# Kernel tuning notes

Measured on AMD Instinct MI355X. Metric: run time of the kernel, lower is better.

The kernel has to match this reference:

```python
import jax, jax.numpy as jnp
import numpy as np

N = 50000
E = 800000
F_IN = 500
H = 5          # heads
C = 32         # per-head channels
HID = H * C    # 160
NC = 20        # num_classes
G = 8          # number of graphs in batch
SLOPE_ATT = 0.2   # GATConv attention leaky slope (PyG default)
SLOPE_ACT = 0.01  # F.leaky_relu default


def _layernorm(x, scale, bias, eps=1e-5):
    mu = jnp.mean(x, axis=-1, keepdims=True)
    var = jnp.var(x, axis=-1, keepdims=True)
    return (x - mu) * jax.lax.rsqrt(var + eps) * scale + bias


def _edge_softmax(logits, dst, num_nodes):
    # segment softmax over incoming edges of each destination node
    m = jax.ops.segment_max(logits, dst, num_segments=num_nodes)
    ex = jnp.exp(logits - m[dst])
    s = jax.ops.segment_sum(ex, dst, num_segments=num_nodes)
    return ex / (s[dst] + 1e-16)


def _gat_layer(x, src, dst, W, a_src, a_dst, b):
    n = x.shape[0]
    h = (x @ W).reshape(n, H, C)                       # [N,H,C]
    al_s = jnp.einsum('nhc,hc->nh', h, a_src)          # [N,H]
    al_d = jnp.einsum('nhc,hc->nh', h, a_dst)
    logits = jax.nn.leaky_relu(al_s[src] + al_d[dst], SLOPE_ATT)  # [Et,H]
    alpha = _edge_softmax(logits, dst, n)              # [Et,H]
    msg = h[src] * alpha[..., None]                    # [Et,H,C]
    out = jax.ops.segment_sum(msg, dst, num_segments=n).reshape(n, HID) + b
    return out, alpha


def setup_inputs():
    key = jax.random.key(0)
    ks = jax.random.split(key, 24)
    p = lambda k, shp: jax.random.normal(k, shp, jnp.float32) * 0.05
    x = jax.random.normal(ks[0], (N, F_IN), jnp.float32)
    edge_index = jax.random.randint(ks[1], (2, E), 0, N, jnp.int64)
    batch = jnp.sort(jax.random.randint(ks[2], (N,), 0, G, jnp.int64))
    return {
        'x': x, 'edge_index': edge_index, 'batch': batch,
        'W1': p(ks[3], (F_IN, HID)), 'a_src1': p(ks[4], (H, C)), 'a_dst1': p(ks[5], (H, C)), 'b1': jnp.zeros((HID,), jnp.float32),
        'ln1_s': jnp.ones((HID,), jnp.float32), 'ln1_b': jnp.zeros((HID,), jnp.float32),
        'W2': p(ks[6], (HID, HID)), 'a_src2': p(ks[7], (H, C)), 'a_dst2': p(ks[8], (H, C)), 'b2': jnp.zeros((HID,), jnp.float32),
        'ln2_s': jnp.ones((HID,), jnp.float32), 'ln2_b': jnp.zeros((HID,), jnp.float32),
        'Wm': p(ks[9], (HID, HID)), 'bm': jnp.zeros((HID,), jnp.float32),
        'Wmlp1': p(ks[10], (HID, HID)), 'bmlp1': jnp.zeros((HID,), jnp.float32),
        'ln3_s': jnp.ones((HID,), jnp.float32), 'ln3_b': jnp.zeros((HID,), jnp.float32),
        'Wmlp2': p(ks[11], (HID, NC)), 'bmlp2': jnp.zeros((NC,), jnp.float32),
    }


def reference(x, edge_index, batch, W1, a_src1, a_dst1, b1, ln1_s, ln1_b,
              W2, a_src2, a_dst2, b2, ln2_s, ln2_b, Wm, bm,
              Wmlp1, bmlp1, ln3_s, ln3_b, Wmlp2, bmlp2):
    n = x.shape[0]
    # PyG GATConv adds self-loops by default
    loops = jnp.arange(n, dtype=edge_index.dtype)
    src = jnp.concatenate([edge_index[0], loops])
    dst = jnp.concatenate([edge_index[1], loops])

    h1, alpha1 = _gat_layer(x, src, dst, W1, a_src1, a_dst1, b1)
    h1 = jax.nn.leaky_relu(h1, SLOPE_ACT)
    h1 = _layernorm(h1, ln1_s, ln1_b)      # dropout = identity at eval

    h2, alpha2 = _gat_layer(h1, src, dst, W2, a_src2, a_dst2, b2)
    h2 = jax.nn.leaky_relu(h2, SLOPE_ACT)
    h2 = _layernorm(h2, ln2_s, ln2_b)

    xo = jax.nn.leaky_relu(h2 @ Wm + bm, SLOPE_ACT)   # [N,HID]

    # global_mean_pool over batch assignment
    sums = jax.ops.segment_sum(xo, batch, num_segments=G)
    cnts = jax.ops.segment_sum(jnp.ones((n, 1), xo.dtype), batch, num_segments=G)
    pooled = sums / jnp.maximum(cnts, 1.0)            # [G,HID]

    z = pooled @ Wmlp1 + bmlp1
    z = jax.nn.relu(_layernorm(z, ln3_s, ln3_b))
    rec = z @ Wmlp2 + bmlp2                           # [G,NC]
    return xo, rec, alpha1, alpha2
```

## Files before the change

kernel.cpp:

```cpp
#include <hip/hip_runtime.h>
#include <hip/hip_bf16.h>
#include <cstdint>
#include <cstddef>

#define NN   50000
#define EE   800000
#define ET_  (EE + NN)
#define FIN  500
#define HID_ 160
#define NC_  20
#define GG   8

typedef __attribute__((ext_vector_type(8))) short ab8;
typedef __attribute__((ext_vector_type(4))) float f4;

static __device__ __forceinline__ unsigned short f2bf(float v) {
    union { float f; uint32_t u; } c; c.f = v;
    uint32_t r = c.u + 0x7FFFu + ((c.u >> 16) & 1u);
    return (unsigned short)(r >> 16);
}

static __device__ __forceinline__ float2 bf2f2(uint32_t u) {
    union { uint32_t u; float f; } a, b;
    a.u = u << 16;
    b.u = u & 0xffff0000u;
    return make_float2(a.f, b.f);
}

static __device__ __forceinline__ int lbound_i(const int* arr, int n, int val) {
    int lo = 0, hi = n;
    while (lo < hi) { int mid = (lo + hi) >> 1; if (arr[mid] < val) lo = mid + 1; else hi = mid; }
    return lo;
}

__global__ __launch_bounds__(256) void k_hist(const int* __restrict__ ei, int* __restrict__ deg) {
    int e = blockIdx.x * 256 + threadIdx.x;
    if (e >= ET_) return;
    int d = (e < EE) ? ei[EE + e] : (e - EE);
    atomicAdd(&deg[d], 1);
}

__global__ __launch_bounds__(256) void k_scan1(const int* __restrict__ deg, int* __restrict__ rowptr,
                                               int* __restrict__ bsum) {
    __shared__ int s[256];
    int t = threadIdx.x;
    int base = blockIdx.x * 1024 + t * 4;
    int v0 = (base + 0 < NN) ? deg[base + 0] : 0;
    int v1 = (base + 1 < NN) ? deg[base + 1] : 0;
    int v2 = (base + 2 < NN) ? deg[base + 2] : 0;
    int v3 = (base + 3 < NN) ? deg[base + 3] : 0;
    int tot = v0 + v1 + v2 + v3;
    s[t] = tot;
    __syncthreads();
    for (int off = 1; off < 256; off <<= 1) {
        int y = (t >= off) ? s[t - off] : 0;
        __syncthreads();
        s[t] += y;
        __syncthreads();
    }
    int excl = s[t] - tot;
    if (t == 255) bsum[blockIdx.x] = s[255];
    if (base + 0 < NN) rowptr[base + 0] = excl;  excl += v0;
    if (base + 1 < NN) rowptr[base + 1] = excl;  excl += v1;
    if (base + 2 < NN) rowptr[base + 2] = excl;  excl += v2;
    if (base + 3 < NN) rowptr[base + 3] = excl;
}

__global__ void k_scan2(int* __restrict__ bsum, int nb) {
    int t = threadIdx.x;
    int v = (t < nb) ? bsum[t] : 0;
    int orig = v;
    for (int off = 1; off < 64; off <<= 1) {
        int y = __shfl_up(v, off);
        if (t >= off) v += y;
    }
    if (t < nb) bsum[t] = v - orig;
}

__global__ __launch_bounds__(256) void k_scan3(int* __restrict__ rowptr, const int* __restrict__ bsum,
                                               int* __restrict__ cursor) {
    int i = blockIdx.x * 256 + threadIdx.x;
    if (i < NN) {
        int r = rowptr[i] + bsum[i >> 10];
        rowptr[i] = r;
        cursor[i] = r;
    }
    if (i == NN) rowptr[NN] = ET_;
}

__global__ __launch_bounds__(256) void k_scatter(const int* __restrict__ ei, int* __restrict__ cursor,
                                                 int2* __restrict__ epair) {
    int e = blockIdx.x * 256 + threadIdx.x;
    if (e >= ET_) return;
    int s, d;
    if (e < EE) { s = ei[e]; d = ei[EE + e]; } else { s = e - EE; d = e - EE; }
    int slot = atomicAdd(&cursor[d], 1);
    epair[slot] = make_int2(e, s);
}

__global__ __launch_bounds__(256) void k_prep_all(const float* __restrict__ W1, unsigned short* __restrict__ Wt1,
                                                  const float* __restrict__ W2, unsigned short* __restrict__ Wt2,
                                                  const float* __restrict__ Wm, unsigned short* __restrict__ Wmt,
                                                  float* __restrict__ pooled) {
    int idx = blockIdx.x * 256 + threadIdx.x;
    const int S1 = HID_ * 512, S2 = HID_ * HID_;
    if (idx < GG * HID_) pooled[idx] = 0.f;
    if (idx < S1) {
        int n = idx / 512, k = idx - n * 512;
        Wt1[idx] = (k < FIN) ? f2bf(W1[(size_t)k * HID_ + n]) : (unsigned short)0;
    } else if (idx < S1 + S2) {
        int j = idx - S1;
        int n = j / HID_, k = j - n * HID_;
        Wt2[j] = f2bf(W2[(size_t)k * HID_ + n]);
    } else if (idx < S1 + 2 * S2) {
        int j = idx - S1 - S2;
        int n = j / HID_, k = j - n * HID_;
        Wmt[j] = f2bf(Wm[(size_t)k * HID_ + n]);
    }
}

template<int ABF>
static __device__ __forceinline__ void gemm_body(const void* __restrict__ Av,
                                                 const unsigned short* __restrict__ Bt,
                                                 float* __restrict__ C, __hip_bfloat16* __restrict__ Cb,
                                                 int M, int K, int Kp,
                                                 const float* __restrict__ bias, int act,
                                                 const float* __restrict__ asrc, const float* __restrict__ adst,
                                                 float* __restrict__ als_o, float* __restrict__ ald_o,
                                                 const int* __restrict__ batch_p, float* __restrict__ pooled) {
    int tid  = threadIdx.x;
    int lane = tid & 63;
    int w    = tid >> 6;
    int fr   = lane & 15;
    int q    = lane >> 4;
    int row0 = blockIdx.x * 64;
    int arow = row0 + w * 16 + fr;
    bool rv  = arow < M;

    f4 acc[10];
#pragma unroll
    for (int t = 0; t < 10; t++) acc[t] = (f4)0.f;

    const int nk = Kp >> 5;
    const unsigned short* bbase = Bt + (size_t)fr * Kp + q * 8;

    auto loadA = [&](int s) -> ab8 {
        ab8 a = (ab8)0;
        int k0 = s * 32 + q * 8;
        if (ABF) {
            const unsigned short* Ab = (const unsigned short*)Av;
            if (rv) a = *reinterpret_cast<const ab8*>(&Ab[(size_t)arow * K + k0]);
        } else {
            const float* A = (const float*)Av;
            if (rv && k0 + 8 <= K) {
                const float4* s4 = reinterpret_cast<const float4*>(&A[(size_t)arow * K + k0]);
                float4 u = s4[0], v = s4[1];
                unsigned short pk[8] = {f2bf(u.x), f2bf(u.y), f2bf(u.z), f2bf(u.w),
                                        f2bf(v.x), f2bf(v.y), f2bf(v.z), f2bf(v.w)};
                a = *reinterpret_cast<ab8*>(pk);
            } else if (rv && k0 < K) {
                unsigned short pk[8];
#pragma unroll
                for (int c = 0; c < 8; c++)
                    pk[c] = (k0 + c < K) ? f2bf(A[(size_t)arow * K + k0 + c]) : (unsigned short)0;
                a = *reinterpret_cast<ab8*>(pk);
            }
        }
        return a;
    };

    ab8 acur = loadA(0);
    for (int s = 0; s < nk; s++) {
        ab8 anx = (ab8)0;
        if (s + 1 < nk) anx = loadA(s + 1);
        const unsigned short* bp = bbase + (size_t)s * 32;
#pragma unroll
        for (int t = 0; t < 10; t++) {
            ab8 b = *reinterpret_cast<const ab8*>(&bp[(size_t)t * 16 * Kp]);
            acc[t] = __builtin_amdgcn_mfma_f32_16x16x32_bf16(acur, b, acc[t], 0, 0, 0);
        }
        acur = anx;
    }

    if (als_o) {
        float av_s[10], av_d[10];
#pragma unroll
        for (int t = 0; t < 10; t++) { av_s[t] = asrc[t * 16 + fr]; av_d[t] = adst[t * 16 + fr]; }
#pragma unroll
        for (int i = 0; i < 4; i++) {
            int r = row0 + w * 16 + q * 4 + i;
            float ps[5], pd[5];
#pragma unroll
            for (int h = 0; h < 5; h++) {
                ps[h] = acc[2 * h][i] * av_s[2 * h] + acc[2 * h + 1][i] * av_s[2 * h + 1];
                pd[h] = acc[2 * h][i] * av_d[2 * h] + acc[2 * h + 1][i] * av_d[2 * h + 1];
            }
#pragma unroll
            for (int off = 8; off >= 1; off >>= 1)
#pragma unroll
                for (int h = 0; h < 5; h++) {
                    ps[h] += __shfl_xor(ps[h], off);
                    pd[h] += __shfl_xor(pd[h], off);
                }
            if (fr == 0 && r < M) {
#pragma unroll
                for (int h = 0; h < 5; h++) {
                    als_o[(size_t)r * 5 + h] = ps[h];
                    ald_o[(size_t)r * 5 + h] = pd[h];
                }
            }
        }
    }

    int gu = -2;
    if (pooled) {
        int rhi = row0 + 63; if (rhi >= M) rhi = M - 1;
        int gl = batch_p[row0], gh = batch_p[rhi];
        gu = (gl == gh) ? gl : -1;
    }
    float psum[10];
#pragma unroll
    for (int t = 0; t < 10; t++) psum[t] = 0.f;

    int rbase = row0 + w * 16 + q * 4;
#pragma unroll
    for (int t = 0; t < 10; t++) {
        int col = t * 16 + fr;
        float bv = bias ? bias[col] : 0.f;
#pragma unroll
        for (int i = 0; i < 4; i++) {
            int r = rbase + i;
            float v = acc[t][i] + bv;
            if (act) v = v > 0.f ? v : 0.01f * v;
            if (r < M) {
                if (C)  C[(size_t)r * HID_ + col] = v;
                if (Cb) *reinterpret_cast<unsigned short*>(&Cb[(size_t)r * HID_ + col]) = f2bf(v);
                if (gu >= 0) psum[t] += v;
                else if (gu == -1) atomicAdd(&pooled[batch_p[r] * HID_ + col], v);
            }
        }
    }
    if (gu >= 0) {
#pragma unroll
        for (int t = 0; t < 10; t++) {
            psum[t] += __shfl_xor(psum[t], 16);
            psum[t] += __shfl_xor(psum[t], 32);
        }
        if (q == 0) {
#pragma unroll
            for (int t = 0; t < 10; t++)
                atomicAdd(&pooled[gu * HID_ + t * 16 + fr], psum[t]);
        }
    }
}

__global__ __launch_bounds__(256) void k_gemm_f32(const void* __restrict__ Av,
                                                  const unsigned short* __restrict__ Bt,
                                                  float* __restrict__ C, __hip_bfloat16* __restrict__ Cb,
                                                  int M, int K, int Kp,
                                                  const float* __restrict__ bias, int act,
                                                  const float* __restrict__ asrc, const float* __restrict__ adst,
                                                  float* __restrict__ als_o, float* __restrict__ ald_o,
                                                  const int* __restrict__ batch_p, float* __restrict__ pooled) {
    gemm_body<0>(Av, Bt, C, Cb, M, K, Kp, bias, act, asrc, adst, als_o, ald_o, batch_p, pooled);
}

__global__ __launch_bounds__(256) void k_gemm_bf16(const void* __restrict__ Av,
                                                   const unsigned short* __restrict__ Bt,
                                                   float* __restrict__ C, __hip_bfloat16* __restrict__ Cb,
                                                   int M, int K, int Kp,
                                                   const float* __restrict__ bias, int act,
                                                   const float* __restrict__ asrc, const float* __restrict__ adst,
                                                   float* __restrict__ als_o, float* __restrict__ ald_o,
                                                   const int* __restrict__ batch_p, float* __restrict__ pooled) {
    gemm_body<1>(Av, Bt, C, Cb, M, K, Kp, bias, act, asrc, adst, als_o, ald_o, batch_p, pooled);
}

__global__ __launch_bounds__(256) void k_att_agg(const int* __restrict__ rowptr,
                                                 const int2* __restrict__ epair,
                                                 const float* __restrict__ als, const float* __restrict__ ald,
                                                 const __hip_bfloat16* __restrict__ hmat,
                                                 float* __restrict__ alphap,
                                                 float* __restrict__ alpha_out,
                                                 const float* __restrict__ bias,
                                                 const float* __restrict__ lns, const float* __restrict__ lnb,
                                                 __hip_bfloat16* __restrict__ outb) {
    __shared__ float sExp[4][64 * 5];
    __shared__ int2  sPair[4][64];
    int wv   = threadIdx.x >> 6;
    int lane = threadIdx.x & 63;
    int node = blockIdx.x * 4 + wv;
    if (node >= NN) return;
    int start = rowptr[node], end = rowptr[node + 1];
    int deg = end - start;
    bool fits = (deg <= 64);
    float ad[5];
#pragma unroll
    for (int h = 0; h < 5; h++) ad[h] = ald[node * 5 + h];

    float sm[5] = {0.f, 0.f, 0.f, 0.f, 0.f};
    for (int j = start + lane; j < end; j += 64) {
        int2 p = epair[j];
        const float* as = &als[(size_t)p.y * 5];
        int idx = j - start;
        if (fits) sPair[wv][idx] = p;
#pragma unroll
        for (int h = 0; h < 5; h++) {
            float l = as[h] + ad[h];
            l = l > 0.f ? l : 0.2f * l;
            float ex = __expf(fminf(l, 60.f));
            sm[h] += ex;
            if (fits) sExp[wv][idx * 5 + h] = ex;
            else      alphap[(size_t)j * 5 + h] = ex;
        }
    }
#pragma unroll
    for (int off = 32; off >= 1; off >>= 1)
#pragma unroll
        for (int h = 0; h < 5; h++) sm[h] += __shfl_xor(sm[h], off);
    float inv[5];
#pragma unroll
    for (int h = 0; h < 5; h++) inv[h] = 1.f / (sm[h] + 1e-16f);

    int h0 = lane >> 4;
    bool lo16 = lane < 16;
    int c01 = 2 * lane;
    int c2  = 128 + 2 * lane;
    float2 A  = make_float2(0.f, 0.f), B2 = make_float2(0.f, 0.f);
    float2 A2 = make_float2(0.f, 0.f), B22 = make_float2(0.f, 0.f);

    if (fits) {
        if (lane < deg) {
            int2 p = sPair[wv][lane];
            float* ao = &alpha_out[(size_t)p.x * 5];
#pragma unroll
            for (int h = 0; h < 5; h++) ao[h] = sExp[wv][lane * 5 + h] * inv[h];
        }
        int idx = 0;
        for (; idx + 1 < deg; idx += 2) {
            int sA = sPair[wv][idx].y, sB = sPair[wv][idx + 1].y;
            float wA = sExp[wv][idx * 5 + h0] * inv[h0];
            float wB = sExp[wv][(idx + 1) * 5 + h0] * inv[h0];
            const unsigned short* rA = (const unsigned short*)&hmat[(size_t)sA * HID_];
            const unsigned short* rB = (const unsigned short*)&hmat[(size_t)sB * HID_];
            float2 fA = bf2f2(*reinterpret_cast<const uint32_t*>(&rA[c01]));
            float2 fB = bf2f2(*reinterpret_cast<const uint32_t*>(&rB[c01]));
            A.x += wA * fA.x; A.y += wA * fA.y;
            B2.x += wB * fB.x; B2.y += wB * fB.y;
            if (lo16) {
                float wA4 = sExp[wv][idx * 5 + 4] * inv[4];
                float wB4 = sExp[wv][(idx + 1) * 5 + 4] * inv[4];
                float2 gA = bf2f2(*reinterpret_cast<const uint32_t*>(&rA[c2]));
                float2 gB = bf2f2(*reinterpret_cast<const uint32_t*>(&rB[c2]));
                A2.x += wA4 * gA.x; A2.y += wA4 * gA.y;
                B22.x += wB4 * gB.x; B22.y += wB4 * gB.y;
            }
        }
        if (idx < deg) {
            int sA = sPair[wv][idx].y;
            float wA = sExp[wv][idx * 5 + h0] * inv[h0];
            const unsigned short* rA = (const unsigned short*)&hmat[(size_t)sA * HID_];
            float2 fA = bf2f2(*reinterpret_cast<const uint32_t*>(&rA[c01]));
            A.x += wA * fA.x; A.y += wA * fA.y;
            if (lo16) {
                float wA4 = sExp[wv][idx * 5 + 4] * inv[4];
                float2 gA = bf2f2(*reinterpret_cast<const uint32_t*>(&rA[c2]));
                A2.x += wA4 * gA.x; A2.y += wA4 * gA.y;
            }
        }
    } else {
        for (int j = start + lane; j < end; j += 64) {
            int2 p = epair[j];
            float* ao = &alpha_out[(size_t)p.x * 5];
#pragma unroll
            for (int h = 0; h < 5; h++) ao[h] = alphap[(size_t)j * 5 + h] * inv[h];
        }
        for (int j = start; j < end; j++) {
            int2 p = epair[j];
            const float* ap = &alphap[(size_t)j * 5];
            float wA = ap[h0] * inv[h0];
            const unsigned short* rA = (const unsigned short*)&hmat[(size_t)p.y * HID_];
            float2 fA = bf2f2(*reinterpret_cast<const uint32_t*>(&rA[c01]));
            A.x += wA * fA.x; A.y += wA * fA.y;
            if (lo16) {
                float wA4 = ap[4] * inv[4];
                float2 gA = bf2f2(*reinterpret_cast<const uint32_t*>(&rA[c2]));
                A2.x += wA4 * gA.x; A2.y += wA4 * gA.y;
            }
        }
    }
    A.x += B2.x; A.y += B2.y; A2.x += B22.x; A2.y += B22.y;

    float2 bb = *reinterpret_cast<const float2*>(&bias[c01]);
    float v0 = A.x + bb.x;  v0 = v0 > 0.f ? v0 : 0.01f * v0;
    float v1 = A.y + bb.y;  v1 = v1 > 0.f ? v1 : 0.01f * v1;
    float v2 = 0.f, v3 = 0.f;
    if (lo16) {
        float2 b2 = *reinterpret_cast<const float2*>(&bias[c2]);
        v2 = A2.x + b2.x; v2 = v2 > 0.f ? v2 : 0.01f * v2;
        v3 = A2.y + b2.y; v3 = v3 > 0.f ? v3 : 0.01f * v3;
    }
    float s  = v0 + v1 + v2 + v3;
    float sq = v0 * v0 + v1 * v1 + v2 * v2 + v3 * v3;
#pragma unroll
    for (int off = 32; off >= 1; off >>= 1) {
        s  += __shfl_xor(s, off);
        sq += __shfl_xor(sq, off);
    }
    float m = s * (1.f / 160.f);
    float r = rsqrtf(sq * (1.f / 160.f) - m * m + 1e-5f);
    size_t ob = (size_t)node * HID_;
    {
        float2 sc = *reinterpret_cast<const float2*>(&lns[c01]);
        float2 bi = *reinterpret_cast<const float2*>(&lnb[c01]);
        uint32_t pk = (uint32_t)f2bf((v0 - m) * r * sc.x + bi.x)
                    | ((uint32_t)f2bf((v1 - m) * r * sc.y + bi.y) << 16);
        *reinterpret_cast<uint32_t*>(&outb[ob + c01]) = pk;
    }
    if (lo16) {
        float2 sc = *reinterpret_cast<const float2*>(&lns[c2]);
        float2 bi = *reinterpret_cast<const float2*>(&lnb[c2]);
        uint32_t pk = (uint32_t)f2bf((v2 - m) * r * sc.x + bi.x)
                    | ((uint32_t)f2bf((v3 - m) * r * sc.y + bi.y) << 16);
        *reinterpret_cast<uint32_t*>(&outb[ob + c2]) = pk;
    }
}

__global__ __launch_bounds__(256) void k_mlp(const float* __restrict__ pooled, const int* __restrict__ batch,
                                             const float* __restrict__ W1, const float* __restrict__ b1,
                                             const float* __restrict__ lns, const float* __restrict__ lnb,
                                             const float* __restrict__ W2, const float* __restrict__ b2,
                                             float* __restrict__ rec) {
    __shared__ float P[GG][HID_];
    __shared__ float Z[GG][HID_];
    __shared__ float mu[GG], rr[GG], ic[GG];
    int t = threadIdx.x;
    if (t < GG) {
        int lo = lbound_i(batch, NN, t), hi = lbound_i(batch, NN, t + 1);
        ic[t] = 1.f / fmaxf((float)(hi - lo), 1.f);
    }
    __syncthreads();
    for (int i = t; i < GG * HID_; i += 256) P[i / HID_][i % HID_] = pooled[i] * ic[i / HID_];
    __syncthreads();
    for (int i = t; i < GG * HID_; i += 256) {
        int g = i / HID_, j = i % HID_;
        float acc = b1[j];
        for (int k = 0; k < HID_; k++) acc += P[g][k] * W1[k * HID_ + j];
        Z[g][j] = acc;
    }
    __syncthreads();
    if (t < GG) {
        float s = 0.f, sq = 0.f;
        for (int k = 0; k < HID_; k++) { float z = Z[t][k]; s += z; sq += z * z; }
        float m = s / (float)HID_;
        mu[t] = m;
        rr[t] = rsqrtf(sq / (float)HID_ - m * m + 1e-5f);
    }
    __syncthreads();
    for (int i = t; i < GG * HID_; i += 256) {
        int g = i / HID_, j = i % HID_;
        float z = (Z[g][j] - mu[g]) * rr[g] * lns[j] + lnb[j];
        Z[g][j] = fmaxf(z, 0.f);
    }
    __syncthreads();
    for (int i = t; i < GG * NC_; i += 256) {
        int g = i / NC_, j = i % NC_;
        float acc = b2[j];
        for (int k = 0; k < HID_; k++) acc += Z[g][k] * W2[k * NC_ + j];
        rec[g * NC_ + j] = acc;
    }
}

extern "C" void kernel_launch(void* const* d_in, const int* in_sizes, int n_in,
                              void* d_out, int out_size, void* d_ws, size_t ws_size,
                              hipStream_t stream) {
    const float* x    = (const float*)d_in[0];
    const int*   ei   = (const int*)d_in[1];
    const int*   batch= (const int*)d_in[2];
    const float* W1   = (const float*)d_in[3];
    const float* as1  = (const float*)d_in[4];
    const float* ad1  = (const float*)d_in[5];
    const float* b1   = (const float*)d_in[6];
    const float* ln1s = (const float*)d_in[7];
    const float* ln1b = (const float*)d_in[8];
    const float* W2   = (const float*)d_in[9];
    const float* as2  = (const float*)d_in[10];
    const float* ad2  = (const float*)d_in[11];
    const float* b2   = (const float*)d_in[12];
    const float* ln2s = (const float*)d_in[13];
    const float* ln2b = (const float*)d_in[14];
    const float* Wm   = (const float*)d_in[15];
    const float* bm   = (const float*)d_in[16];
    const float* Wm1  = (const float*)d_in[17];
    const float* bm1  = (const float*)d_in[18];
    const float* ln3s = (const float*)d_in[19];
    const float* ln3b = (const float*)d_in[20];
    const float* Wm2  = (const float*)d_in[21];
    const float* bm2  = (const float*)d_in[22];

    float* out    = (float*)d_out;
    float* xo     = out;
    float* rec    = out + (size_t)NN * HID_;
    float* alpha1 = rec + GG * NC_;
    float* alpha2 = alpha1 + (size_t)ET_ * 5;

    char* w = (char*)d_ws;
    auto carve = [&](size_t bytes) { char* p = w; w += (bytes + 255) & ~(size_t)255; return p; };
    int*   deg    = (int*)carve((size_t)NN * 4);
    int*   rowptr = (int*)carve((size_t)(NN + 1) * 4);
    int*   cursor = (int*)carve((size_t)NN * 4);
    int2*  epair  = (int2*)carve((size_t)ET_ * 8);
    int*   bsum   = (int*)carve(64 * 4);
    __hip_bfloat16* hbuf  = (__hip_bfloat16*)carve((size_t)NN * HID_ * 2);
    __hip_bfloat16* xbufb = (__hip_bfloat16*)carve((size_t)NN * HID_ * 2);
    float* alphap = (float*)carve((size_t)ET_ * 5 * 4);
    float* als    = (float*)carve((size_t)NN * 5 * 4);
    float* ald    = (float*)carve((size_t)NN * 5 * 4);
    float* pooled = (float*)carve((size_t)GG * HID_ * 4);
    unsigned short* Wt1 = (unsigned short*)carve((size_t)HID_ * 512 * 2);
    unsigned short* Wt2 = (unsigned short*)carve((size_t)HID_ * HID_ * 2);
    unsigned short* Wmt = (unsigned short*)carve((size_t)HID_ * HID_ * 2);

    hipMemsetAsync(deg, 0, (size_t)NN * 4, stream);
    k_hist<<<(ET_ + 255) / 256, 256, 0, stream>>>(ei, deg);
    int nb = (NN + 1023) / 1024;
    k_scan1<<<nb, 256, 0, stream>>>(deg, rowptr, bsum);
    k_scan2<<<1, 64, 0, stream>>>(bsum, nb);
    k_scan3<<<(NN + 1 + 255) / 256, 256, 0, stream>>>(rowptr, bsum, cursor);
    k_scatter<<<(ET_ + 255) / 256, 256, 0, stream>>>(ei, cursor, epair);

    const int PREP = HID_ * 512 + 2 * HID_ * HID_;
    k_prep_all<<<(PREP + 255) / 256, 256, 0, stream>>>(W1, Wt1, W2, Wt2, Wm, Wmt, pooled);

    const int NWB = (NN + 3) / 4;
    const int GB  = (NN + 63) / 64;

    k_gemm_f32<<<GB, 256, 0, stream>>>(x, Wt1, nullptr, hbuf, NN, FIN, 512, nullptr, 0,
                                       as1, ad1, als, ald, nullptr, nullptr);
    k_att_agg<<<NWB, 256, 0, stream>>>(rowptr, epair, als, ald, hbuf, alphap, alpha1,
                                       b1, ln1s, ln1b, xbufb);

    k_gemm_bf16<<<GB, 256, 0, stream>>>(xbufb, Wt2, nullptr, hbuf, NN, HID_, HID_, nullptr, 0,
                                        as2, ad2, als, ald, nullptr, nullptr);
    k_att_agg<<<NWB, 256, 0, stream>>>(rowptr, epair, als, ald, hbuf, alphap, alpha2,
                                       b2, ln2s, ln2b, xbufb);

    k_gemm_bf16<<<GB, 256, 0, stream>>>(xbufb, Wmt, xo, nullptr, NN, HID_, HID_, bm, 1,
                                        nullptr, nullptr, nullptr, nullptr, batch, pooled);
    k_mlp<<<1, 256, 0, stream>>>(pooled, batch, Wm1, bm1, ln3s, ln3b, Wm2, bm2, rec);
}
```

Baseline: 717.0 us.

## Pre-pack weights and input into MFMA fragment order with deeper prefetch

Weights are repacked into MFMA fragment order so each lane does one coalesced 16-byte load per tile. The fp32 input x is converted to bf16 in a separate kernel, also in fragment order, staged in the output buffer. The GEMM main loop now double-buffers B fragments in registers and prefetches A two steps ahead. This removes strided B loads and in-loop fp32 conversion, but adds an extra pass over x, register pressure and a scratch dependency on d_out before xo is written.

```diff
diff --git a/kernel.cpp b/kernel.cpp
--- a/kernel.cpp
+++ b/kernel.cpp
@@ -10,6 +10,9 @@
 #define HID_ 160
 #define NC_  20
 #define GG   8
+#define GB1  ((NN + 63) / 64)
+#define NK1  16
+#define NK2  5
 
 typedef __attribute__((ext_vector_type(8))) short ab8;
 typedef __attribute__((ext_vector_type(4))) float f4;
@@ -98,32 +101,64 @@
     epair[slot] = make_int2(e, s);
 }
 
-__global__ __launch_bounds__(256) void k_prep_all(const float* __restrict__ W1, unsigned short* __restrict__ Wt1,
-                                                  const float* __restrict__ W2, unsigned short* __restrict__ Wt2,
-                                                  const float* __restrict__ Wm, unsigned short* __restrict__ Wmt,
+__global__ __launch_bounds__(256) void k_prep_all(const float* __restrict__ W1, ab8* __restrict__ B1,
+                                                  const float* __restrict__ W2, ab8* __restrict__ B2,
+                                                  const float* __restrict__ Wm, ab8* __restrict__ Bm,
                                                   float* __restrict__ pooled) {
     int idx = blockIdx.x * 256 + threadIdx.x;
-    const int S1 = HID_ * 512, S2 = HID_ * HID_;
     if (idx < GG * HID_) pooled[idx] = 0.f;
-    if (idx < S1) {
-        int n = idx / 512, k = idx - n * 512;
-        Wt1[idx] = (k < FIN) ? f2bf(W1[(size_t)k * HID_ + n]) : (unsigned short)0;
-    } else if (idx < S1 + S2) {
-        int j = idx - S1;
-        int n = j / HID_, k = j - n * HID_;
-        Wt2[j] = f2bf(W2[(size_t)k * HID_ + n]);
-    } else if (idx < S1 + 2 * S2) {
-        int j = idx - S1 - S2;
-        int n = j / HID_, k = j - n * HID_;
-        Wmt[j] = f2bf(Wm[(size_t)k * HID_ + n]);
-    }
-}
-
-template<int ABF>
+    const int C1 = NK1 * 10 * 64;
+    const int C2 = NK2 * 10 * 64;
+    const float* W; ab8* Bo; int K, cidx;
+    if (idx < C1)                { W = W1; Bo = B1; K = FIN;  cidx = idx; }
+    else if (idx < C1 + C2)      { W = W2; Bo = B2; K = HID_; cidx = idx - C1; }
+    else if (idx < C1 + 2 * C2)  { W = Wm; Bo = Bm; K = HID_; cidx = idx - C1 - C2; }
+    else return;
+    int s = cidx / 640, r = cidx % 640;
+    int t = r >> 6, l = r & 63;
+    int fr = l & 15, q = l >> 4;
+    int n  = t * 16 + fr;
+    int k0 = s * 32 + q * 8;
+    unsigned short pk[8];
+#pragma unroll
+    for (int j = 0; j < 8; j++) {
+        int k = k0 + j;
+        pk[j] = (k < K) ? f2bf(W[(size_t)k * HID_ + n]) : (unsigned short)0;
+    }
+    Bo[cidx] = *reinterpret_cast<ab8*>(pk);
+}
+
+__global__ __launch_bounds__(256) void k_conv_x(const float* __restrict__ x, ab8* __restrict__ Apk) {
+    int idx = blockIdx.x * 256 + threadIdx.x;
+    int tid = idx & 255;
+    int s   = (idx >> 8) & (NK1 - 1);
+    int blk = idx >> 12;
+    int l = tid & 63, w = tid >> 6;
+    int fr = l & 15, q = l >> 4;
+    int row = blk * 64 + w * 16 + fr;
+    int k0 = s * 32 + q * 8;
+    unsigned short pk[8] = {0, 0, 0, 0, 0, 0, 0, 0};
+    if (row < NN) {
+        const float* xr = &x[(size_t)row * FIN];
+        if (k0 + 8 <= FIN) {
+            const float4* s4 = reinterpret_cast<const float4*>(&xr[k0]);
+            float4 u = s4[0], v = s4[1];
+            pk[0] = f2bf(u.x); pk[1] = f2bf(u.y); pk[2] = f2bf(u.z); pk[3] = f2bf(u.w);
+            pk[4] = f2bf(v.x); pk[5] = f2bf(v.y); pk[6] = f2bf(v.z); pk[7] = f2bf(v.w);
+        } else {
+#pragma unroll
+            for (int j = 0; j < 8; j++)
+                if (k0 + j < FIN) pk[j] = f2bf(xr[k0 + j]);
+        }
+    }
+    Apk[idx] = *reinterpret_cast<ab8*>(pk);
+}
+
+template<int PKA>
 static __device__ __forceinline__ void gemm_body(const void* __restrict__ Av,
-                                                 const unsigned short* __restrict__ Bt,
+                                                 const ab8* __restrict__ Bpk, int nk,
                                                  float* __restrict__ C, __hip_bfloat16* __restrict__ Cb,
-                                                 int M, int K, int Kp,
+                                                 int M, int K,
                                                  const float* __restrict__ bias, int act,
                                                  const float* __restrict__ asrc, const float* __restrict__ adst,
                                                  float* __restrict__ als_o, float* __restrict__ ald_o,
@@ -141,45 +176,35 @@
 #pragma unroll
     for (int t = 0; t < 10; t++) acc[t] = (f4)0.f;
 
-    const int nk = Kp >> 5;
-    const unsigned short* bbase = Bt + (size_t)fr * Kp + q * 8;
+    const ab8* bb  = Bpk + lane;
+    const ab8* apk = reinterpret_cast<const ab8*>(Av) + (size_t)blockIdx.x * nk * 256 + tid;
+    const unsigned short* Arow = (const unsigned short*)Av;
 
     auto loadA = [&](int s) -> ab8 {
+        if (PKA) return apk[s * 256];
         ab8 a = (ab8)0;
-        int k0 = s * 32 + q * 8;
-        if (ABF) {
-            const unsigned short* Ab = (const unsigned short*)Av;
-            if (rv) a = *reinterpret_cast<const ab8*>(&Ab[(size_t)arow * K + k0]);
-        } else {
-            const float* A = (const float*)Av;
-            if (rv && k0 + 8 <= K) {
-                const float4* s4 = reinterpret_cast<const float4*>(&A[(size_t)arow * K + k0]);
-                float4 u = s4[0], v = s4[1];
-                unsigned short pk[8] = {f2bf(u.x), f2bf(u.y), f2bf(u.z), f2bf(u.w),
-                                        f2bf(v.x), f2bf(v.y), f2bf(v.z), f2bf(v.w)};
-                a = *reinterpret_cast<ab8*>(pk);
-            } else if (rv && k0 < K) {
-                unsigned short pk[8];
-#pragma unroll
-                for (int c = 0; c < 8; c++)
-                    pk[c] = (k0 + c < K) ? f2bf(A[(size_t)arow * K + k0 + c]) : (unsigned short)0;
-                a = *reinterpret_cast<ab8*>(pk);
-            }
-        }
+        if (rv) a = *reinterpret_cast<const ab8*>(&Arow[(size_t)arow * K + s * 32 + q * 8]);
         return a;
     };
 
-    ab8 acur = loadA(0);
+    ab8 bcur[10], bnx[10];
+#pragma unroll
+    for (int t = 0; t < 10; t++) bcur[t] = bb[t * 64];
+    ab8 a0 = loadA(0);
+    ab8 a1 = loadA(1);
     for (int s = 0; s < nk; s++) {
-        ab8 anx = (ab8)0;
-        if (s + 1 < nk) anx = loadA(s + 1);
-        const unsigned short* bp = bbase + (size_t)s * 32;
-#pragma unroll
-        for (int t = 0; t < 10; t++) {
-            ab8 b = *reinterpret_cast<const ab8*>(&bp[(size_t)t * 16 * Kp]);
-            acc[t] = __builtin_amdgcn_mfma_f32_16x16x32_bf16(acur, b, acc[t], 0, 0, 0);
-        }
-        acur = anx;
+        if (s + 1 < nk) {
+#pragma unroll
+            for (int t = 0; t < 10; t++) bnx[t] = bb[((s + 1) * 10 + t) * 64];
+        }
+        ab8 a2 = (ab8)0;
+        if (s + 2 < nk) a2 = loadA(s + 2);
+#pragma unroll
+        for (int t = 0; t < 10; t++)
+            acc[t] = __builtin_amdgcn_mfma_f32_16x16x32_bf16(a0, bcur[t], acc[t], 0, 0, 0);
+        a0 = a1; a1 = a2;
+#pragma unroll
+        for (int t = 0; t < 10; t++) bcur[t] = bnx[t];
     }
 
     if (als_o) {
@@ -254,26 +279,26 @@
     }
 }
 
-__global__ __launch_bounds__(256) void k_gemm_f32(const void* __restrict__ Av,
-                                                  const unsigned short* __restrict__ Bt,
-                                                  float* __restrict__ C, __hip_bfloat16* __restrict__ Cb,
-                                                  int M, int K, int Kp,
-                                                  const float* __restrict__ bias, int act,
-                                                  const float* __restrict__ asrc, const float* __restrict__ adst,
-                                                  float* __restrict__ als_o, float* __restrict__ ald_o,
-                                                  const int* __restrict__ batch_p, float* __restrict__ pooled) {
-    gemm_body<0>(Av, Bt, C, Cb, M, K, Kp, bias, act, asrc, adst, als_o, ald_o, batch_p, pooled);
-}
-
-__global__ __launch_bounds__(256) void k_gemm_bf16(const void* __restrict__ Av,
-                                                   const unsigned short* __restrict__ Bt,
-                                                   float* __restrict__ C, __hip_bfloat16* __restrict__ Cb,
-                                                   int M, int K, int Kp,
-                                                   const float* __restrict__ bias, int act,
-                                                   const float* __restrict__ asrc, const float* __restrict__ adst,
-                                                   float* __restrict__ als_o, float* __restrict__ ald_o,
-                                                   const int* __restrict__ batch_p, float* __restrict__ pooled) {
-    gemm_body<1>(Av, Bt, C, Cb, M, K, Kp, bias, act, asrc, adst, als_o, ald_o, batch_p, pooled);
+__global__ __launch_bounds__(256) void k_gemm_pk(const void* __restrict__ Av,
+                                                 const ab8* __restrict__ Bpk, int nk,
+                                                 float* __restrict__ C, __hip_bfloat16* __restrict__ Cb,
+                                                 int M, int K,
+                                                 const float* __restrict__ bias, int act,
+                                                 const float* __restrict__ asrc, const float* __restrict__ adst,
+                                                 float* __restrict__ als_o, float* __restrict__ ald_o,
+                                                 const int* __restrict__ batch_p, float* __restrict__ pooled) {
+    gemm_body<1>(Av, Bpk, nk, C, Cb, M, K, bias, act, asrc, adst, als_o, ald_o, batch_p, pooled);
+}
+
+__global__ __launch_bounds__(256) void k_gemm_rm(const void* __restrict__ Av,
+                                                 const ab8* __restrict__ Bpk, int nk,
+                                                 float* __restrict__ C, __hip_bfloat16* __restrict__ Cb,
+                                                 int M, int K,
+                                                 const float* __restrict__ bias, int act,
+                                                 const float* __restrict__ asrc, const float* __restrict__ adst,
+                                                 float* __restrict__ als_o, float* __restrict__ ald_o,
+                                                 const int* __restrict__ batch_p, float* __restrict__ pooled) {
+    gemm_body<0>(Av, Bpk, nk, C, Cb, M, K, bias, act, asrc, adst, als_o, ald_o, batch_p, pooled);
 }
 
 __global__ __launch_bounds__(256) void k_att_agg(const int* __restrict__ rowptr,
@@ -517,9 +542,10 @@
     float* als    = (float*)carve((size_t)NN * 5 * 4);
     float* ald    = (float*)carve((size_t)NN * 5 * 4);
     float* pooled = (float*)carve((size_t)GG * HID_ * 4);
-    unsigned short* Wt1 = (unsigned short*)carve((size_t)HID_ * 512 * 2);
-    unsigned short* Wt2 = (unsigned short*)carve((size_t)HID_ * HID_ * 2);
-    unsigned short* Wmt = (unsigned short*)carve((size_t)HID_ * HID_ * 2);
+    ab8*   B1pk   = (ab8*)carve((size_t)NK1 * 10 * 64 * 16);
+    ab8*   B2pk   = (ab8*)carve((size_t)NK2 * 10 * 64 * 16);
+    ab8*   Bmpk   = (ab8*)carve((size_t)NK2 * 10 * 64 * 16);
+    ab8*   Apk    = (ab8*)d_out;
 
     hipMemsetAsync(deg, 0, (size_t)NN * 4, stream);
     k_hist<<<(ET_ + 255) / 256, 256, 0, stream>>>(ei, deg);
@@ -529,23 +555,23 @@
     k_scan3<<<(NN + 1 + 255) / 256, 256, 0, stream>>>(rowptr, bsum, cursor);
     k_scatter<<<(ET_ + 255) / 256, 256, 0, stream>>>(ei, cursor, epair);
 
-    const int PREP = HID_ * 512 + 2 * HID_ * HID_;
-    k_prep_all<<<(PREP + 255) / 256, 256, 0, stream>>>(W1, Wt1, W2, Wt2, Wm, Wmt, pooled);
+    const int PREP = NK1 * 10 * 64 + 2 * NK2 * 10 * 64;
+    k_prep_all<<<(PREP + 255) / 256, 256, 0, stream>>>(W1, B1pk, W2, B2pk, Wm, Bmpk, pooled);
+    k_conv_x<<<GB1 * NK1, 256, 0, stream>>>(x, Apk);
 
     const int NWB = (NN + 3) / 4;
-    const int GB  = (NN + 63) / 64;
-
-    k_gemm_f32<<<GB, 256, 0, stream>>>(x, Wt1, nullptr, hbuf, NN, FIN, 512, nullptr, 0,
+
+    k_gemm_pk<<<GB1, 256, 0, stream>>>(Apk, B1pk, NK1, nullptr, hbuf, NN, FIN, nullptr, 0,
                                        as1, ad1, als, ald, nullptr, nullptr);
     k_att_agg<<<NWB, 256, 0, stream>>>(rowptr, epair, als, ald, hbuf, alphap, alpha1,
                                        b1, ln1s, ln1b, xbufb);
 
-    k_gemm_bf16<<<GB, 256, 0, stream>>>(xbufb, Wt2, nullptr, hbuf, NN, HID_, HID_, nullptr, 0,
-                                        as2, ad2, als, ald, nullptr, nullptr);
+    k_gemm_rm<<<GB1, 256, 0, stream>>>(xbufb, B2pk, NK2, nullptr, hbuf, NN, HID_, nullptr, 0,
+                                       as2, ad2, als, ald, nullptr, nullptr);
     k_att_agg<<<NWB, 256, 0, stream>>>(rowptr, epair, als, ald, hbuf, alphap, alpha2,
                                        b2, ln2s, ln2b, xbufb);
 
-    k_gemm_bf16<<<GB, 256, 0, stream>>>(xbufb, Wmt, xo, nullptr, NN, HID_, HID_, bm, 1,
-                                        nullptr, nullptr, nullptr, nullptr, batch, pooled);
+    k_gemm_rm<<<GB1, 256, 0, stream>>>(xbufb, Bmpk, NK2, xo, nullptr, NN, HID_, bm, 1,
+                                       nullptr, nullptr, nullptr, nullptr, batch, pooled);
     k_mlp<<<1, 256, 0, stream>>>(pooled, batch, Wm1, bm1, ln3s, ln3b, Wm2, bm2, rec);
 }
```

Measured after the change: 647.4 us. 9.7% less time.
